# Kernel optimization log

Measured on AMD Instinct MI355X. Metric: run time of the kernel, lower is better.

Reference implementation:

```python
import jax, jax.numpy as jnp
import numpy as np

B, S, D, P, NQ = 8, 2048, 1024, 256, 8192


def setup_inputs() -> dict:
    key = jax.random.key(0)
    ks = jax.random.split(key, 8)
    return {
        "flag": 0,
        "encoded_input": jax.random.normal(ks[0], (B, S, D), dtype=jnp.float32),
        "start_ids_1": jax.random.randint(ks[1], (NQ,), 0, S, dtype=jnp.int32),
        "end_ids_1": jax.random.randint(ks[2], (NQ,), 0, S, dtype=jnp.int32),
        "query_batch_idx": jax.random.randint(ks[3], (NQ,), 0, B, dtype=jnp.int32),
        "start_ids_2": jax.random.randint(ks[4], (NQ,), 0, S, dtype=jnp.int32),
        "end_ids_2": jax.random.randint(ks[5], (NQ,), 0, S, dtype=jnp.int32),
        "W": jax.random.normal(ks[6], (D, P), dtype=jnp.float32) * 0.02,
        "b": jnp.zeros((P,), dtype=jnp.float32),
    }


def _gather_spans(h, qb, s, e):
    # span_repr[b, i, j] = concat(h[b, i], h[b, j]) for j >= i, else 0.
    # Direct gather instead of building the O(seq^2) table.
    rep = jnp.concatenate([h[qb, s], h[qb, e]], axis=-1)  # [NQ, 2*P]
    valid = (e >= s).astype(rep.dtype)[:, None]
    return rep * valid


def reference(flag, encoded_input, start_ids_1, end_ids_1, query_batch_idx,
              start_ids_2, end_ids_2, W, b):
    h = encoded_input @ W + b  # [B, S, P] (use_proj=True)
    res1 = _gather_spans(h, query_batch_idx, start_ids_1, end_ids_1)
    res2 = _gather_spans(h, query_batch_idx, start_ids_2, end_ids_2)
    return (res1, res2)
```

## Files before the change

### kernel.cpp

```cpp
#include <hip/hip_runtime.h>
#include <hip/hip_bf16.h>
#include <stdint.h>

#define S_LEN 2048
#define D_DIM 1024
#define P_DIM 256
#define NQ_   8192
#define M_TOT 16384

#define BM 32
#define BN 256
#define BK 64

typedef __attribute__((ext_vector_type(4))) float  f32x4;
typedef __attribute__((ext_vector_type(8))) __bf16 bf16x8;
typedef __attribute__((ext_vector_type(4))) __bf16 bf16x4;

__device__ __forceinline__ void async16(const void* g, void* l) {
    __builtin_amdgcn_global_load_lds(
        (const __attribute__((address_space(1))) uint32_t*)g,
        (__attribute__((address_space(3))) uint32_t*)l, 16, 0, 0);
}

__global__ __launch_bounds__(1024) void wt_kernel(const float* __restrict__ W,
                                                  __bf16* __restrict__ WT) {
    __shared__ __bf16 tile[32][33];
    const int k0 = blockIdx.x * 32;
    const int n0 = blockIdx.y * 32;
    const int tx = threadIdx.x, ty = threadIdx.y;
    tile[ty][tx] = (__bf16)W[(k0 + ty) * P_DIM + (n0 + tx)];
    __syncthreads();
    WT[(n0 + ty) * D_DIM + (k0 + tx)] = tile[tx][ty];
}

__global__ __launch_bounds__(256, 2) void gemm_kernel(const float*  __restrict__ A,
                                                      const __bf16* __restrict__ WT,
                                                      const float*  __restrict__ bias,
                                                      float*        __restrict__ H) {
    __shared__ __bf16 As[2][BM * BK];
    __shared__ __bf16 Bs[2][BN * BK];

    const int tid = threadIdx.x;
    const int w   = tid >> 6;
    const int l   = tid & 63;
    const int lm  = l & 15;
    const int q   = l >> 4;

    const int m0 = blockIdx.x * BM;

    const int brow_l = l >> 3;
    const int bc     = (l & 7) ^ (brow_l & 7);
    const __bf16* bg0 = WT + (size_t)(w * 64 + brow_l * 1) * 0;

    auto stageB = [&](int buf, int k0) {
        #pragma unroll
        for (int j = 0; j < 8; ++j) {
            const int r   = w * 8 + j;
            const int row = r * 8 + brow_l;
            const __bf16* g = WT + (size_t)row * D_DIM + k0 + bc * 8;
            async16(g, &Bs[buf][r * 512]);
        }
    };

    const int arow = tid >> 3;
    const int acp  = tid & 7;
    const int ac   = acp ^ (arow & 7);
    const float* agp = A + (size_t)(m0 + arow) * D_DIM + ac * 8;

    float4 fa0, fa1;
    auto loadA = [&](int k0) {
        fa0 = *(const float4*)(agp + k0);
        fa1 = *(const float4*)(agp + k0 + 4);
    };
    auto writeA = [&](int buf) {
        bf16x8 v;
        v[0] = (__bf16)fa0.x; v[1] = (__bf16)fa0.y; v[2] = (__bf16)fa0.z; v[3] = (__bf16)fa0.w;
        v[4] = (__bf16)fa1.x; v[5] = (__bf16)fa1.y; v[6] = (__bf16)fa1.z; v[7] = (__bf16)fa1.w;
        *(bf16x8*)(&As[buf][arow * BK + acp * 8]) = v;
    };

    f32x4 acc[2][4] = {};

    auto compute = [&](int buf) {
        #pragma unroll
        for (int kh = 0; kh < 2; ++kh) {
            const int pos = ((kh * 4 + q) ^ (lm & 7)) * 8;
            bf16x8 af[2], bfr[4];
            #pragma unroll
            for (int mi = 0; mi < 2; ++mi)
                af[mi] = *(const bf16x8*)(&As[buf][(mi * 16 + lm) * BK + pos]);
            #pragma unroll
            for (int ni = 0; ni < 4; ++ni)
                bfr[ni] = *(const bf16x8*)(&Bs[buf][(w * 64 + ni * 16 + lm) * BK + pos]);
            #pragma unroll
            for (int mi = 0; mi < 2; ++mi)
                #pragma unroll
                for (int ni = 0; ni < 4; ++ni)
                    acc[mi][ni] = __builtin_amdgcn_mfma_f32_16x16x32_bf16(
                        af[mi], bfr[ni], acc[mi][ni], 0, 0, 0);
        }
    };

    loadA(0);
    stageB(0, 0);
    writeA(0);
    __syncthreads();

    #pragma unroll 1
    for (int p = 0; p < 7; ++p) {
        const int k1 = (2 * p + 1) * BK, k2 = (2 * p + 2) * BK;
        loadA(k1); stageB(1, k1);
        __builtin_amdgcn_sched_barrier(0);
        compute(0);
        __builtin_amdgcn_sched_barrier(0);
        writeA(1);
        __syncthreads();
        loadA(k2); stageB(0, k2);
        __builtin_amdgcn_sched_barrier(0);
        compute(1);
        __builtin_amdgcn_sched_barrier(0);
        writeA(0);
        __syncthreads();
    }
    {
        const int k1 = 15 * BK;
        loadA(k1); stageB(1, k1);
        __builtin_amdgcn_sched_barrier(0);
        compute(0);
        __builtin_amdgcn_sched_barrier(0);
        writeA(1);
        __syncthreads();
    }
    compute(1);

    #pragma unroll
    for (int ni = 0; ni < 4; ++ni) {
        const int col = w * 64 + ni * 16 + lm;
        const float bv = bias[col];
        #pragma unroll
        for (int mi = 0; mi < 2; ++mi) {
            const int rbase = m0 + mi * 16 + q * 4;
            #pragma unroll
            for (int r = 0; r < 4; ++r)
                H[(size_t)(rbase + r) * P_DIM + col] = acc[mi][ni][r] + bv;
        }
    }
}

__global__ __launch_bounds__(256) void gather_kernel(const float* __restrict__ H,
                                                     const int* __restrict__ s1,
                                                     const int* __restrict__ e1,
                                                     const int* __restrict__ qb,
                                                     const int* __restrict__ s2,
                                                     const int* __restrict__ e2,
                                                     float* __restrict__ out) {
    const int qi  = blockIdx.x;
    const int t   = threadIdx.x;
    const int b   = qb[qi];
    const int set = t >> 7;
    const int rem = t & 127;
    const int half = rem >> 6;
    const int c4  = (rem & 63) << 2;

    const int s = set ? s2[qi] : s1[qi];
    const int e = set ? e2[qi] : e1[qi];

    float4 v = make_float4(0.f, 0.f, 0.f, 0.f);
    if (e >= s) {
        const int ridx = half ? e : s;
        v = *(const float4*)(H + ((size_t)b * S_LEN + ridx) * P_DIM + c4);
    }
    *(float4*)(out + (size_t)set * (NQ_ * 512) + (size_t)qi * 512 + half * 256 + c4) = v;
}

extern "C" void kernel_launch(void* const* d_in, const int* in_sizes, int n_in,
                              void* d_out, int out_size, void* d_ws, size_t ws_size,
                              hipStream_t stream) {
    const float* A    = (const float*)d_in[1];
    const int*   s1   = (const int*)  d_in[2];
    const int*   e1   = (const int*)  d_in[3];
    const int*   qb   = (const int*)  d_in[4];
    const int*   s2   = (const int*)  d_in[5];
    const int*   e2   = (const int*)  d_in[6];
    const float* W    = (const float*)d_in[7];
    const float* bias = (const float*)d_in[8];
    float*       out  = (float*)d_out;

    __bf16* WT = (__bf16*)d_ws;
    float*  H  = (float*)((char*)d_ws + (1 << 20));

    wt_kernel    <<<dim3(32, 8), dim3(32, 32), 0, stream>>>(W, WT);
    gemm_kernel  <<<dim3(M_TOT / BM), dim3(256), 0, stream>>>(A, WT, bias, H);
    gather_kernel<<<dim3(NQ_), dim3(256), 0, stream>>>(H, s1, e1, qb, s2, e2, out);
}
```

Baseline: 146.3 us.

## Load A fragments directly into registers, store H as bf16, restructure gather

The GEMM no longer stages the fp32 activation tile through LDS. Each lane loads its MFMA A-fragment directly from global memory into double-buffered registers and converts it to bf16 inside compute. The intermediate H is now written in bf16, which halves its write and read traffic at some precision cost. The gather is rewritten so each wave handles 8 query rows, reading both span endpoints and writing output with nontemporal stores from 512 blocks instead of 8192.

```diff
diff --git a/kernel.cpp b/kernel.cpp
--- a/kernel.cpp
+++ b/kernel.cpp
@@ -22,6 +22,10 @@
         (__attribute__((address_space(3))) uint32_t*)l, 16, 0, 0);
 }
 
+__device__ __forceinline__ void nts(f32x4 v, float* p) {
+    __builtin_nontemporal_store(v, (f32x4*)p);
+}
+
 __global__ __launch_bounds__(1024) void wt_kernel(const float* __restrict__ W,
                                                   __bf16* __restrict__ WT) {
     __shared__ __bf16 tile[32][33];
@@ -36,8 +40,7 @@
 __global__ __launch_bounds__(256, 2) void gemm_kernel(const float*  __restrict__ A,
                                                       const __bf16* __restrict__ WT,
                                                       const float*  __restrict__ bias,
-                                                      float*        __restrict__ H) {
-    __shared__ __bf16 As[2][BM * BK];
+                                                      __bf16*       __restrict__ H) {
     __shared__ __bf16 Bs[2][BN * BK];
 
     const int tid = threadIdx.x;
@@ -50,48 +53,49 @@
 
     const int brow_l = l >> 3;
     const int bc     = (l & 7) ^ (brow_l & 7);
-    const __bf16* bg0 = WT + (size_t)(w * 64 + brow_l * 1) * 0;
 
     auto stageB = [&](int buf, int k0) {
         #pragma unroll
         for (int j = 0; j < 8; ++j) {
             const int r   = w * 8 + j;
             const int row = r * 8 + brow_l;
-            const __bf16* g = WT + (size_t)row * D_DIM + k0 + bc * 8;
-            async16(g, &Bs[buf][r * 512]);
+            async16(WT + (size_t)row * D_DIM + k0 + bc * 8, &Bs[buf][r * 512]);
         }
     };
 
-    const int arow = tid >> 3;
-    const int acp  = tid & 7;
-    const int ac   = acp ^ (arow & 7);
-    const float* agp = A + (size_t)(m0 + arow) * D_DIM + ac * 8;
+    const float* ap0 = A + (size_t)(m0 + lm)      * D_DIM + q * 8;
+    const float* ap1 = A + (size_t)(m0 + 16 + lm) * D_DIM + q * 8;
 
-    float4 fa0, fa1;
-    auto loadA = [&](int k0) {
-        fa0 = *(const float4*)(agp + k0);
-        fa1 = *(const float4*)(agp + k0 + 4);
-    };
-    auto writeA = [&](int buf) {
-        bf16x8 v;
-        v[0] = (__bf16)fa0.x; v[1] = (__bf16)fa0.y; v[2] = (__bf16)fa0.z; v[3] = (__bf16)fa0.w;
-        v[4] = (__bf16)fa1.x; v[5] = (__bf16)fa1.y; v[6] = (__bf16)fa1.z; v[7] = (__bf16)fa1.w;
-        *(bf16x8*)(&As[buf][arow * BK + acp * 8]) = v;
+    f32x4 acc[2][4] = {};
+    float4 ra0[2][2][2];
+    float4 ra1[2][2][2];
+
+    auto loadA = [&](float4 (&ra)[2][2][2], int k0) {
+        #pragma unroll
+        for (int kh = 0; kh < 2; ++kh) {
+            ra[0][kh][0] = *(const float4*)(ap0 + k0 + kh * 32);
+            ra[0][kh][1] = *(const float4*)(ap0 + k0 + kh * 32 + 4);
+            ra[1][kh][0] = *(const float4*)(ap1 + k0 + kh * 32);
+            ra[1][kh][1] = *(const float4*)(ap1 + k0 + kh * 32 + 4);
+        }
     };
 
-    f32x4 acc[2][4] = {};
-
-    auto compute = [&](int buf) {
+    auto compute = [&](const float4 (&ra)[2][2][2], int buf) {
         #pragma unroll
         for (int kh = 0; kh < 2; ++kh) {
             const int pos = ((kh * 4 + q) ^ (lm & 7)) * 8;
-            bf16x8 af[2], bfr[4];
-            #pragma unroll
-            for (int mi = 0; mi < 2; ++mi)
-                af[mi] = *(const bf16x8*)(&As[buf][(mi * 16 + lm) * BK + pos]);
+            bf16x8 bfr[4];
             #pragma unroll
             for (int ni = 0; ni < 4; ++ni)
                 bfr[ni] = *(const bf16x8*)(&Bs[buf][(w * 64 + ni * 16 + lm) * BK + pos]);
+            bf16x8 af[2];
+            #pragma unroll
+            for (int mi = 0; mi < 2; ++mi) {
+                af[mi][0] = (__bf16)ra[mi][kh][0].x; af[mi][1] = (__bf16)ra[mi][kh][0].y;
+                af[mi][2] = (__bf16)ra[mi][kh][0].z; af[mi][3] = (__bf16)ra[mi][kh][0].w;
+                af[mi][4] = (__bf16)ra[mi][kh][1].x; af[mi][5] = (__bf16)ra[mi][kh][1].y;
+                af[mi][6] = (__bf16)ra[mi][kh][1].z; af[mi][7] = (__bf16)ra[mi][kh][1].w;
+            }
             #pragma unroll
             for (int mi = 0; mi < 2; ++mi)
                 #pragma unroll
@@ -101,37 +105,27 @@
         }
     };
 
-    loadA(0);
+    loadA(ra0, 0);
     stageB(0, 0);
-    writeA(0);
     __syncthreads();
 
     #pragma unroll 1
-    for (int p = 0; p < 7; ++p) {
-        const int k1 = (2 * p + 1) * BK, k2 = (2 * p + 2) * BK;
-        loadA(k1); stageB(1, k1);
+    for (int ph = 0; ph < 7; ++ph) {
+        const int k1 = (2 * ph + 1) * BK, k2 = (2 * ph + 2) * BK;
+        loadA(ra1, k1); stageB(1, k1);
         __builtin_amdgcn_sched_barrier(0);
-        compute(0);
+        compute(ra0, 0);
+        __syncthreads();
+        loadA(ra0, k2); stageB(0, k2);
         __builtin_amdgcn_sched_barrier(0);
-        writeA(1);
-        __syncthreads();
-        loadA(k2); stageB(0, k2);
-        __builtin_amdgcn_sched_barrier(0);
-        compute(1);
-        __builtin_amdgcn_sched_barrier(0);
-        writeA(0);
+        compute(ra1, 1);
         __syncthreads();
     }
-    {
-        const int k1 = 15 * BK;
-        loadA(k1); stageB(1, k1);
-        __builtin_amdgcn_sched_barrier(0);
-        compute(0);
-        __builtin_amdgcn_sched_barrier(0);
-        writeA(1);
-        __syncthreads();
-    }
-    compute(1);
+    loadA(ra1, 15 * BK); stageB(1, 15 * BK);
+    __builtin_amdgcn_sched_barrier(0);
+    compute(ra0, 0);
+    __syncthreads();
+    compute(ra1, 1);
 
     #pragma unroll
     for (int ni = 0; ni < 4; ++ni) {
@@ -142,35 +136,41 @@
             const int rbase = m0 + mi * 16 + q * 4;
             #pragma unroll
             for (int r = 0; r < 4; ++r)
-                H[(size_t)(rbase + r) * P_DIM + col] = acc[mi][ni][r] + bv;
+                H[(size_t)(rbase + r) * P_DIM + col] = (__bf16)(acc[mi][ni][r] + bv);
         }
     }
 }
 
-__global__ __launch_bounds__(256) void gather_kernel(const float* __restrict__ H,
+__global__ __launch_bounds__(256) void gather_kernel(const __bf16* __restrict__ H,
                                                      const int* __restrict__ s1,
                                                      const int* __restrict__ e1,
                                                      const int* __restrict__ qb,
                                                      const int* __restrict__ s2,
                                                      const int* __restrict__ e2,
                                                      float* __restrict__ out) {
-    const int qi  = blockIdx.x;
-    const int t   = threadIdx.x;
-    const int b   = qb[qi];
-    const int set = t >> 7;
-    const int rem = t & 127;
-    const int half = rem >> 6;
-    const int c4  = (rem & 63) << 2;
+    const int wave = (blockIdx.x * 256 + threadIdx.x) >> 6;
+    const int l    = threadIdx.x & 63;
 
-    const int s = set ? s2[qi] : s1[qi];
-    const int e = set ? e2[qi] : e1[qi];
+    #pragma unroll
+    for (int j = 0; j < 8; ++j) {
+        const int p   = wave * 8 + j;
+        const int set = p >> 13;
+        const int qi  = p & 8191;
+        const int s   = set ? s2[qi] : s1[qi];
+        const int e   = set ? e2[qi] : e1[qi];
+        const int b   = qb[qi];
 
-    float4 v = make_float4(0.f, 0.f, 0.f, 0.f);
-    if (e >= s) {
-        const int ridx = half ? e : s;
-        v = *(const float4*)(H + ((size_t)b * S_LEN + ridx) * P_DIM + c4);
+        f32x4 v0 = {0.f, 0.f, 0.f, 0.f}, v1 = v0;
+        if (e >= s) {
+            const bf16x4 a = *(const bf16x4*)(H + ((size_t)b * S_LEN + s) * P_DIM + l * 4);
+            const bf16x4 c = *(const bf16x4*)(H + ((size_t)b * S_LEN + e) * P_DIM + l * 4);
+            v0[0] = (float)a[0]; v0[1] = (float)a[1]; v0[2] = (float)a[2]; v0[3] = (float)a[3];
+            v1[0] = (float)c[0]; v1[1] = (float)c[1]; v1[2] = (float)c[2]; v1[3] = (float)c[3];
+        }
+        float* op = out + (size_t)set * (NQ_ * 512) + (size_t)qi * 512;
+        nts(v0, op + l * 4);
+        nts(v1, op + 256 + l * 4);
     }
-    *(float4*)(out + (size_t)set * (NQ_ * 512) + (size_t)qi * 512 + half * 256 + c4) = v;
 }
 
 extern "C" void kernel_launch(void* const* d_in, const int* in_sizes, int n_in,
@@ -187,9 +187,9 @@
     float*       out  = (float*)d_out;
 
     __bf16* WT = (__bf16*)d_ws;
-    float*  H  = (float*)((char*)d_ws + (1 << 20));
+    __bf16* H  = (__bf16*)((char*)d_ws + (1 << 20));
 
     wt_kernel    <<<dim3(32, 8), dim3(32, 32), 0, stream>>>(W, WT);
     gemm_kernel  <<<dim3(M_TOT / BM), dim3(256), 0, stream>>>(A, WT, bias, H);
-    gather_kernel<<<dim3(NQ_), dim3(256), 0, stream>>>(H, s1, e1, qb, s2, e2, out);
+    gather_kernel<<<dim3(512), dim3(256), 0, stream>>>(H, s1, e1, qb, s2, e2, out);
 }
```

Measured after the change: 163.8 us. 1.12x slower.
